# Optimization experiments

Hardware: AMD Instinct MI355X
Metric: run time of the kernel (lower is better)

## Reference

```python
import jax, jax.numpy as jnp
import numpy as np

B, L, D, H = 2, 2048, 2048, 16
DH = D // H

def setup_inputs() -> dict:
    key = jax.random.key(0)
    ks = jax.random.split(key, 7)
    q = jax.random.normal(ks[0], (B, L, D), dtype=jnp.float32)
    k = jax.random.normal(ks[1], (B, L, D), dtype=jnp.float32)
    v = jax.random.normal(ks[2], (B, L, D), dtype=jnp.float32)
    # causal mask: True means masked (matches torch masked_fill semantics)
    attn_mask = jnp.triu(jnp.ones((L, L), dtype=bool), k=1)[None, None, :, :]
    scale = 0.02
    wq = jax.random.normal(ks[3], (D, D), dtype=jnp.float32) * scale
    wk = jax.random.normal(ks[4], (D, D), dtype=jnp.float32) * scale
    wv = jax.random.normal(ks[5], (D, D), dtype=jnp.float32) * scale
    wo = jax.random.normal(ks[6], (D, D), dtype=jnp.float32) * scale
    return {"q": q, "k": k, "v": v, "attn_mask": attn_mask,
            "wq": wq, "wk": wk, "wv": wv, "wo": wo}

def _split_heads(x):
    b, l, _ = x.shape
    return x.reshape(b, l, H, DH).transpose(0, 2, 1, 3)  # [B,H,L,DH]

def reference(q, k, v, attn_mask, wq, wk, wv, wo):
    # torch Linear: y = x @ W.T (bias=False)
    qh = _split_heads(q @ wq.T)
    kh = _split_heads(k @ wk.T)
    vh = _split_heads(v @ wv.T)
    scale = 1.0 / np.sqrt(DH).astype(np.float32)
    scores = jnp.einsum('bhqd,bhkd->bhqk', qh, kh) * scale
    neg = jnp.finfo(scores.dtype).min
    scores = jnp.where(attn_mask, neg, scores)
    attn = jax.nn.softmax(scores, axis=-1)
    ctx = jnp.einsum('bhqk,bhkd->bhqd', attn, vh)
    ctx = ctx.transpose(0, 2, 1, 3).reshape(q.shape[0], q.shape[1], D)
    return ctx @ wo.T
```

## Files before the change

kernel.cpp:

```cpp
#include <hip/hip_runtime.h>

#define B_  2
#define L_  2048
#define D_  2048
#define H_  16
#define DH_ 128
#define K_  2048

typedef __attribute__((ext_vector_type(8))) short bf16x8;
typedef __attribute__((ext_vector_type(4))) float f32x4;
typedef __attribute__((ext_vector_type(4))) float float4v;
typedef __attribute__((ext_vector_type(8))) unsigned short u16x8;
typedef __attribute__((ext_vector_type(4))) unsigned short u16x4;

__device__ __forceinline__ unsigned short f2bf(float f) {
  unsigned u = __builtin_bit_cast(unsigned, f);
  u += 0x7fffu + ((u >> 16) & 1u);
  return (unsigned short)(u >> 16);
}

typedef __attribute__((address_space(3))) unsigned int lds_uint;
typedef __attribute__((address_space(1))) const unsigned int glob_uint;
__device__ __forceinline__ void gld16(const void* g, void* l) {
  __builtin_amdgcn_global_load_lds((glob_uint*)g, (lds_uint*)l, 16, 0, 0);
}

#define BAR() do { asm volatile("" ::: "memory"); __builtin_amdgcn_s_barrier(); asm volatile("" ::: "memory"); } while (0)
#define VMCNT(n) asm volatile("s_waitcnt vmcnt(" #n ")" ::: "memory")

__global__ void cvt_all(const float* __restrict__ wq, const float* __restrict__ wk,
                        const float* __restrict__ wv, const float* __restrict__ wo,
                        const float* __restrict__ q, const float* __restrict__ k,
                        const float* __restrict__ v, unsigned short* __restrict__ ws,
                        int nacts) {
  const size_t DD = (size_t)D_ * D_;
  const size_t BLD = (size_t)B_ * L_ * D_;
  const int z = blockIdx.z;
  const float* src;
  unsigned short* dst;
  size_t nelem;
  if (z < 4) {
    src = (z == 0) ? wq : (z == 1) ? wk : (z == 2) ? wv : wo;
    dst = ws + (size_t)z * DD;
    nelem = DD;
  } else {
    if (z - 4 >= nacts) return;
    src = (z == 4) ? q : (z == 5) ? k : v;
    dst = ws + 4 * DD + (size_t)(z - 4) * BLD;
    nelem = BLD;
  }
  size_t i = ((size_t)blockIdx.x * 256 + threadIdx.x) * 8;
  if (i >= nelem) return;
  float4v x0 = *(const float4v*)(src + i);
  float4v x1 = *(const float4v*)(src + i + 4);
  u16x8 p;
  p[0]=f2bf(x0[0]); p[1]=f2bf(x0[1]); p[2]=f2bf(x0[2]); p[3]=f2bf(x0[3]);
  p[4]=f2bf(x1[0]); p[5]=f2bf(x1[1]); p[6]=f2bf(x1[2]); p[7]=f2bf(x1[3]);
  *(u16x8*)(dst + i) = p;
}

template <int KIND>
__global__ __launch_bounds__(512, 2) void gemm8(
    const unsigned short* __restrict__ a0, const unsigned short* __restrict__ a1,
    const unsigned short* __restrict__ a2,
    const unsigned short* __restrict__ w0, const unsigned short* __restrict__ w1,
    const unsigned short* __restrict__ w2,
    unsigned short* __restrict__ Qh, unsigned short* __restrict__ Kh,
    unsigned short* __restrict__ Vt, float* __restrict__ OF) {
  __shared__ unsigned short smem[3 * 24576];

  const int lin = blockIdx.x + 32 * (blockIdx.y + 8 * blockIdx.z);
  const int cpx = KIND ? 32 : 96;
  const int s = (lin & 7) * cpx + (lin >> 3);
  const int mt = s & 31;
  const int r_ = s >> 5;
  const int ntile = KIND ? r_ : (r_ & 7);
  const int z = KIND ? 0 : (r_ >> 3);

  const unsigned short* A = KIND ? a0 : (z == 0 ? a0 : z == 1 ? a1 : a2);
  const unsigned short* W = KIND ? w0 : (z == 0 ? w0 : z == 1 ? w1 : w2);
  const int mode = KIND ? 2 : (z == 2 ? 1 : 0);

  const int bm0 = mt * 128;
  const int bn0 = ntile * 256;

  const int tid = threadIdx.x;
  const int wid = tid >> 6, lane = tid & 63;
  const int wr = wid >> 2, wc = wid & 3;
  const int l15 = lane & 15, l4 = lane >> 4;

  const unsigned short* gsrc[6];
  int ldst[6];
  {
#pragma unroll
    for (int i = 0; i < 2; ++i) {
      const int c = i * 512 + tid, r = c >> 3, s0 = c & 7;
      gsrc[i] = A + (size_t)(bm0 + r) * K_ + ((s0 ^ (r & 7)) << 3);
      ldst[i] = c * 8;
    }
#pragma unroll
    for (int u = 0; u < 2; ++u)
#pragma unroll
      for (int i = 0; i < 2; ++i) {
        const int c = i * 512 + tid, r = c >> 3, s0 = c & 7;
        gsrc[2 + u * 2 + i] = W + (size_t)(bn0 + u * 128 + r) * K_ + ((s0 ^ (r & 7)) << 3);
        ldst[2 + u * 2 + i] = 8192 + (u * 1024 + c) * 8;
      }
  }
#define STAGE(idx, p) do { gld16(gsrc[idx], &smem[(p) * 24576 + ldst[idx]]); gsrc[idx] += 64; } while (0)

  int offA[4][2], offB[4][2];
#pragma unroll
  for (int mf = 0; mf < 4; ++mf)
#pragma unroll
    for (int ks = 0; ks < 2; ++ks) {
      const int row = wr * 64 + mf * 16 + l15;
      const int ch = ks * 4 + l4;
      offA[mf][ks] = row * 64 + ((ch ^ (row & 7)) << 3);
    }
#pragma unroll
  for (int nf = 0; nf < 4; ++nf)
#pragma unroll
    for (int ks = 0; ks < 2; ++ks) {
      const int rowb = wc * 64 + nf * 16 + l15;
      const int ch = ks * 4 + l4;
      offB[nf][ks] = 8192 + rowb * 64 + ((ch ^ (rowb & 7)) << 3);
    }

  f32x4 acc[4][4];
#pragma unroll
  for (int m = 0; m < 4; ++m)
#pragma unroll
    for (int n = 0; n < 4; ++n) { f32x4 zz = {0.f, 0.f, 0.f, 0.f}; acc[m][n] = zz; }

  STAGE(0, 0); STAGE(1, 0); STAGE(2, 0); STAGE(3, 0); STAGE(4, 0); STAGE(5, 0);
  STAGE(0, 1); STAGE(1, 1); STAGE(2, 1); STAGE(3, 1); STAGE(4, 1); STAGE(5, 1);
  VMCNT(6);
  BAR();

  int p = 0;
  for (int t = 0; t < 32; ++t) {
    int p2 = p + 2; if (p2 >= 3) p2 -= 3;
    const unsigned short* bA = &smem[p * 24576];
    bf16x8 af[4][2], bfr[4][2];
#pragma unroll
    for (int mf = 0; mf < 4; ++mf)
#pragma unroll
      for (int ks = 0; ks < 2; ++ks)
        af[mf][ks] = *(const bf16x8*)&bA[offA[mf][ks]];
#pragma unroll
    for (int nf = 0; nf < 4; ++nf)
#pragma unroll
      for (int ks = 0; ks < 2; ++ks)
        bfr[nf][ks] = *(const bf16x8*)&bA[offB[nf][ks]];
    if (t < 30) { STAGE(0, p2); STAGE(1, p2); STAGE(2, p2); STAGE(3, p2); STAGE(4, p2); STAGE(5, p2); }
    __builtin_amdgcn_s_setprio(1);
#pragma unroll
    for (int mf = 0; mf < 4; ++mf)
#pragma unroll
      for (int nf = 0; nf < 4; ++nf)
#pragma unroll
        for (int ks = 0; ks < 2; ++ks)
          acc[mf][nf] = __builtin_amdgcn_mfma_f32_16x16x32_bf16(af[mf][ks], bfr[nf][ks], acc[mf][nf], 0, 0, 0);
    __builtin_amdgcn_s_setprio(0);
    if (t < 30) { VMCNT(6); } else { VMCNT(0); }
    BAR();
    p = (p == 2) ? 0 : p + 1;
  }
#undef STAGE

  if (mode == 0) {
    unsigned short* O = (z == 0) ? Qh : Kh;
#pragma unroll
    for (int mf = 0; mf < 4; ++mf) {
      const int rr = bm0 + wr * 64 + mf * 16 + l4 * 4;
#pragma unroll
      for (int nf = 0; nf < 4; ++nf) {
        const int cc = bn0 + wc * 64 + nf * 16 + l15;
        const int h = cc >> 7, dh = cc & 127;
#pragma unroll
        for (int j = 0; j < 4; ++j) {
          const int r2 = rr + j;
          O[((size_t)((r2 >> 11) * H_ + h) * L_ + (r2 & 2047)) * DH_ + dh] = f2bf(acc[mf][nf][j]);
        }
      }
    }
  } else if (mode == 1) {
    unsigned short* T = smem;
#pragma unroll
    for (int mf = 0; mf < 4; ++mf) {
      const int rl = wr * 64 + mf * 16 + l4 * 4;
#pragma unroll
      for (int nf = 0; nf < 4; ++nf) {
        const int cl = wc * 64 + nf * 16 + l15;
        u16x4 vv;
#pragma unroll
        for (int j = 0; j < 4; ++j) vv[j] = f2bf(acc[mf][nf][j]);
        *(u16x4*)&T[cl * 136 + rl] = vv;
      }
    }
    __syncthreads();
    const int b = bm0 >> 11, lbase = bm0 & 2047;
#pragma unroll
    for (int it = 0; it < 8; ++it) {
      const int idx = it * 512 + tid;
      const int rT = idx >> 4, cT = idx & 15;
      u16x8 val = *(const u16x8*)&T[rT * 136 + cT * 8];
      const int n = bn0 + rT, h = n >> 7, dh = n & 127;
      *(u16x8*)&Vt[((size_t)(b * H_ + h) * DH_ + dh) * L_ + lbase + cT * 8] = val;
    }
  } else {
#pragma unroll
    for (int mf = 0; mf < 4; ++mf) {
      const int rr = bm0 + wr * 64 + mf * 16 + l4 * 4;
#pragma unroll
      for (int nf = 0; nf < 4; ++nf) {
        const int cc = bn0 + wc * 64 + nf * 16 + l15;
#pragma unroll
        for (int j = 0; j < 4; ++j) OF[(size_t)(rr + j) * D_ + cc] = acc[mf][nf][j];
      }
    }
  }
}

__global__ __launch_bounds__(256, 2) void proj_gemm_f32a(
    const float* __restrict__ q, const float* __restrict__ k, const float* __restrict__ v,
    const unsigned short* __restrict__ wqb, const unsigned short* __restrict__ wkb,
    const unsigned short* __restrict__ wvb,
    unsigned short* __restrict__ Qh, unsigned short* __restrict__ Kh,
    unsigned short* __restrict__ Vt) {
  __shared__ unsigned short smem[128 * 136];
  unsigned short* As = smem;
  unsigned short* Bs = smem + 128 * 64;

  const int z = blockIdx.z;
  const float* A = (z == 0) ? q : (z == 1) ? k : v;
  const unsigned short* W = (z == 0) ? wqb : (z == 1) ? wkb : wvb;

  const int tid = threadIdx.x;
  const int wave = tid >> 6, lane = tid & 63;
  const int wr = wave >> 1, wc = wave & 1;
  const int bm0 = blockIdx.x * 128;
  const int bn0 = blockIdx.y * 128;
  const int l15 = lane & 15, l4 = lane >> 4;

  f32x4 acc[4][4];
#pragma unroll
  for (int m = 0; m < 4; m++)
#pragma unroll
    for (int n = 0; n < 4; n++) { f32x4 zz = {0.f, 0.f, 0.f, 0.f}; acc[m][n] = zz; }

  for (int k0 = 0; k0 < K_; k0 += 64) {
#pragma unroll
    for (int it = 0; it < 4; ++it) {
      const int base = it * 256 + wave * 64;
      const int ch = base + lane;
      const int r = ch >> 3, c = ch & 7;
      gld16(W + (size_t)(bn0 + r) * K_ + (k0 + c * 8), Bs + base * 8);
    }
#pragma unroll
    for (int it = 0; it < 4; ++it) {
      const int ch = it * 256 + tid;
      const int r = ch >> 3, c = ch & 7;
      const float* g = A + (size_t)(bm0 + r) * K_ + (k0 + c * 8);
      float4v x0 = *(const float4v*)g;
      float4v x1 = *(const float4v*)(g + 4);
      u16x8 pp;
      pp[0]=f2bf(x0[0]); pp[1]=f2bf(x0[1]); pp[2]=f2bf(x0[2]); pp[3]=f2bf(x0[3]);
      pp[4]=f2bf(x1[0]); pp[5]=f2bf(x1[1]); pp[6]=f2bf(x1[2]); pp[7]=f2bf(x1[3]);
      *(u16x8*)&As[ch * 8] = pp;
    }
    __syncthreads();
#pragma unroll
    for (int ks = 0; ks < 2; ++ks) {
      const int kc = ks * 32 + l4 * 8;
      bf16x8 af[4], bfr[4];
#pragma unroll
      for (int m = 0; m < 4; m++) af[m] = *(const bf16x8*)&As[(wr * 64 + m * 16 + l15) * 64 + kc];
#pragma unroll
      for (int n = 0; n < 4; n++) bfr[n] = *(const bf16x8*)&Bs[(wc * 64 + n * 16 + l15) * 64 + kc];
#pragma unroll
      for (int m = 0; m < 4; m++)
#pragma unroll
        for (int n = 0; n < 4; n++)
          acc[m][n] = __builtin_amdgcn_mfma_f32_16x16x32_bf16(af[m], bfr[n], acc[m][n], 0, 0, 0);
    }
    __syncthreads();
  }

  if (z < 2) {
    unsigned short* O = (z == 0) ? Qh : Kh;
#pragma unroll
    for (int m = 0; m < 4; m++) {
      const int rr = bm0 + wr * 64 + m * 16 + l4 * 4;
#pragma unroll
      for (int n = 0; n < 4; n++) {
        const int cc = bn0 + wc * 64 + n * 16 + l15;
        const int h = cc >> 7, dh = cc & 127;
#pragma unroll
        for (int j = 0; j < 4; j++) {
          const int r2 = rr + j;
          O[((size_t)((r2 >> 11) * H_ + h) * L_ + (r2 & 2047)) * DH_ + dh] = f2bf(acc[m][n][j]);
        }
      }
    }
  } else {
    __syncthreads();
    unsigned short* T = smem;
#pragma unroll
    for (int m = 0; m < 4; m++)
#pragma unroll
      for (int n = 0; n < 4; n++) {
        const int cl = wc * 64 + n * 16 + l15;
        const int rl = wr * 64 + m * 16 + l4 * 4;
#pragma unroll
        for (int j = 0; j < 4; j++) T[cl * 136 + rl + j] = f2bf(acc[m][n][j]);
      }
    __syncthreads();
    const int b = bm0 >> 11, lbase = bm0 & 2047;
    const int hb = bn0 >> 7;
#pragma unroll
    for (int it = 0; it < 8; ++it) {
      const int idx = it * 256 + tid;
      const int dhl = idx >> 4, c = idx & 15;
      u16x8 val = *(const u16x8*)&T[dhl * 136 + c * 8];
      *(u16x8*)&Vt[((size_t)(b * H_ + hb) * DH_ + dhl) * L_ + lbase + c * 8] = val;
    }
  }
}

#define SCALE_ 0.08838834764831845f

__global__ __launch_bounds__(512, 2) void attn_kernel(
    const unsigned short* __restrict__ Qh, const unsigned short* __restrict__ Kh,
    const unsigned short* __restrict__ Vt, unsigned short* __restrict__ ctx) {
  __shared__ unsigned short Ks[128 * 128];
  __shared__ unsigned short Vs[128 * 128];
  __shared__ unsigned short Ps[8][16 * 128];

  const int pair = blockIdx.x, bh = blockIdx.y;
  const size_t hoff = (size_t)bh * L_ * DH_;
  const unsigned short* Qp = Qh + hoff;
  const unsigned short* Kp = Kh + hoff;
  const unsigned short* Vp = Vt + hoff;

  const int tid = threadIdx.x, wave = tid >> 6, lane = tid & 63;
  const int l15 = lane & 15, l4 = lane >> 4;
  const int b = bh >> 4, h = bh & 15;

#pragma unroll 1
  for (int p = 0; p < 2; ++p) {
    const int qt = p ? (15 - pair) : pair;
    const int ntiles = qt + 1;

    bf16x8 qf[4];
    {
      const int qrow = qt * 128 + wave * 16 + l15;
#pragma unroll
      for (int s = 0; s < 4; s++)
        qf[s] = *(const bf16x8*)&Qp[(size_t)qrow * DH_ + s * 32 + l4 * 8];
    }

    f32x4 o[8];
#pragma unroll
    for (int df = 0; df < 8; df++) { f32x4 zz = {0.f, 0.f, 0.f, 0.f}; o[df] = zz; }
    float m_r[4] = {-1e30f, -1e30f, -1e30f, -1e30f};
    float l_r[4] = {0.f, 0.f, 0.f, 0.f};

    for (int kt = 0; kt < ntiles; ++kt) {
#pragma unroll
      for (int it = 0; it < 4; ++it) {
        const int ch = it * 512 + tid;
        const int r = ch >> 4, s = ch & 15;
        gld16(Kp + (size_t)(kt * 128 + r) * DH_ + ((s ^ (r & 7)) * 8), (unsigned short*)Ks + ch * 8);
      }
#pragma unroll
      for (int it = 0; it < 4; ++it) {
        const int ch = it * 512 + tid;
        const int r = ch >> 4, s = ch & 15;
        gld16(Vp + (size_t)r * L_ + kt * 128 + ((s ^ (r & 7)) * 8), (unsigned short*)Vs + ch * 8);
      }
      __syncthreads();

      f32x4 sa[8];
#pragma unroll
      for (int f = 0; f < 8; f++) { f32x4 zz = {0.f, 0.f, 0.f, 0.f}; sa[f] = zz; }
      __builtin_amdgcn_s_setprio(1);
#pragma unroll
      for (int ks = 0; ks < 4; ++ks) {
        const int c = ks * 4 + l4;
#pragma unroll
        for (int f = 0; f < 8; ++f) {
          const int n = f * 16 + l15;
          bf16x8 kf = *(const bf16x8*)&Ks[n * 128 + ((c ^ (n & 7)) * 8)];
          sa[f] = __builtin_amdgcn_mfma_f32_16x16x32_bf16(qf[ks], kf, sa[f], 0, 0, 0);
        }
      }
      __builtin_amdgcn_s_setprio(0);

      const bool last = (kt == qt);
#pragma unroll
      for (int f = 0; f < 8; f++) {
        const int kg = kt * 128 + f * 16 + l15;
#pragma unroll
        for (int j = 0; j < 4; j++) {
          float t = sa[f][j] * SCALE_;
          if (last && kg > qt * 128 + wave * 16 + l4 * 4 + j) t = -1e30f;
          sa[f][j] = t;
        }
      }

#pragma unroll
      for (int j = 0; j < 4; j++) {
        float mx = fmaxf(fmaxf(fmaxf(sa[0][j], sa[1][j]), fmaxf(sa[2][j], sa[3][j])),
                         fmaxf(fmaxf(sa[4][j], sa[5][j]), fmaxf(sa[6][j], sa[7][j])));
#pragma unroll
        for (int d = 1; d < 16; d <<= 1) mx = fmaxf(mx, __shfl_xor(mx, d));
        const float mnew = fmaxf(m_r[j], mx);
        const float alpha = __expf(m_r[j] - mnew);
        float rs = 0.f;
        const int row = l4 * 4 + j;
#pragma unroll
        for (int f = 0; f < 8; f++) {
          float pp = __expf(sa[f][j] - mnew);
          rs += pp;
          const int col = f * 16 + l15;
          const int c = col >> 3;
          Ps[wave][row * 128 + ((c ^ (row & 7)) * 8) + (col & 7)] = f2bf(pp);
        }
#pragma unroll
        for (int d = 1; d < 16; d <<= 1) rs += __shfl_xor(rs, d);
        l_r[j] = l_r[j] * alpha + rs;
        m_r[j] = mnew;
#pragma unroll
        for (int df = 0; df < 8; df++) o[df][j] *= alpha;
      }

      __builtin_amdgcn_s_setprio(1);
#pragma unroll
      for (int ksl = 0; ksl < 4; ++ksl) {
        const int pc = ksl * 4 + l4;
        bf16x8 pf = *(const bf16x8*)&Ps[wave][l15 * 128 + ((pc ^ (l15 & 7)) * 8)];
#pragma unroll
        for (int df = 0; df < 8; ++df) {
          const int vr = df * 16 + l15;
          bf16x8 vf = *(const bf16x8*)&Vs[vr * 128 + ((pc ^ (vr & 7)) * 8)];
          o[df] = __builtin_amdgcn_mfma_f32_16x16x32_bf16(pf, vf, o[df], 0, 0, 0);
        }
      }
      __builtin_amdgcn_s_setprio(0);
      __syncthreads();
    }

#pragma unroll
    for (int j = 0; j < 4; j++) {
      const float inv = 1.0f / l_r[j];
      const int lq = qt * 128 + wave * 16 + l4 * 4 + j;
      const size_t rowb = ((size_t)(b * L_ + lq)) * D_ + h * DH_;
#pragma unroll
      for (int df = 0; df < 8; ++df)
        ctx[rowb + df * 16 + l15] = f2bf(o[df][j] * inv);
    }
  }
}

extern "C" void kernel_launch(void* const* d_in, const int* in_sizes, int n_in,
                              void* d_out, int out_size, void* d_ws, size_t ws_size,
                              hipStream_t stream) {
  const float* q  = (const float*)d_in[0];
  const float* k  = (const float*)d_in[1];
  const float* v  = (const float*)d_in[2];
  const float* wq = (const float*)d_in[4];
  const float* wk = (const float*)d_in[5];
  const float* wv = (const float*)d_in[6];
  const float* wo = (const float*)d_in[7];

  const size_t DD = (size_t)D_ * D_;
  const size_t BLD = (size_t)B_ * L_ * D_;
  unsigned short* ws  = (unsigned short*)d_ws;
  unsigned short* wqb = ws;
  unsigned short* wkb = wqb + DD;
  unsigned short* wvb = wkb + DD;
  unsigned short* wob = wvb + DD;

  const size_t need_full = (4 * DD + 7 * BLD) * 2;

  if (ws_size >= need_full) {
    unsigned short* qb  = wob + DD;
    unsigned short* kb  = qb + BLD;
    unsigned short* vb  = kb + BLD;
    unsigned short* QhP = vb + BLD;
    unsigned short* KhP = QhP + BLD;
    unsigned short* VtP = KhP + BLD;
    unsigned short* ctx = VtP + BLD;

    cvt_all<<<dim3(4096, 1, 7), 256, 0, stream>>>(wq, wk, wv, wo, q, k, v, ws, 3);
    gemm8<0><<<dim3(32, 8, 3), 512, 0, stream>>>(qb, kb, vb, wqb, wkb, wvb, QhP, KhP, VtP, nullptr);
    attn_kernel<<<dim3(8, 32), 512, 0, stream>>>(QhP, KhP, VtP, ctx);
    gemm8<1><<<dim3(32, 8, 1), 512, 0, stream>>>(ctx, nullptr, nullptr, wob, nullptr, nullptr,
                                                 nullptr, nullptr, nullptr, (float*)d_out);
  } else {
    unsigned short* QhP = wob + DD;
    unsigned short* KhP = QhP + BLD;
    unsigned short* VtP = KhP + BLD;
    unsigned short* ctx = VtP + BLD;

    cvt_all<<<dim3(4096, 1, 4), 256, 0, stream>>>(wq, wk, wv, wo, q, k, v, ws, 0);
    proj_gemm_f32a<<<dim3(32, 16, 3), 256, 0, stream>>>(q, k, v, wqb, wkb, wvb, QhP, KhP, VtP);
    attn_kernel<<<dim3(8, 32), 512, 0, stream>>>(QhP, KhP, VtP, ctx);
    gemm8<1><<<dim3(32, 8, 1), 512, 0, stream>>>(ctx, nullptr, nullptr, wob, nullptr, nullptr,
                                                 nullptr, nullptr, nullptr, (float*)d_out);
  }
}
```

Baseline: 286.5 us.

## Use 256x256 tiles with double buffering for QKV projection GEMM

Replaces the templated 128x256 triple-buffered projection GEMM with a dedicated 256x256-tile kernel that uses two LDS buffers of 64 KB each. Each wave now computes an 8x4 grid of MFMA fragments, loading A fragments inside the loop to limit register pressure. The V transpose epilogue is split into two halves so it fits in shared memory. The larger tile raises arithmetic intensity and cuts global traffic, but it halves the grid to 384 blocks, needs more registers for the bigger accumulator, and waits on VMCNT(0) each iteration, which reduces load/compute overlap. The output projection moves into its own non-templated kernel.

```diff
diff --git a/kernel.cpp b/kernel.cpp
--- a/kernel.cpp
+++ b/kernel.cpp
@@ -59,27 +59,165 @@
   *(u16x8*)(dst + i) = p;
 }
 
-template <int KIND>
-__global__ __launch_bounds__(512, 2) void gemm8(
+__global__ __launch_bounds__(512, 2) void gemm256(
     const unsigned short* __restrict__ a0, const unsigned short* __restrict__ a1,
     const unsigned short* __restrict__ a2,
     const unsigned short* __restrict__ w0, const unsigned short* __restrict__ w1,
     const unsigned short* __restrict__ w2,
     unsigned short* __restrict__ Qh, unsigned short* __restrict__ Kh,
-    unsigned short* __restrict__ Vt, float* __restrict__ OF) {
+    unsigned short* __restrict__ Vt) {
+  __shared__ unsigned short smem[2 * 32768];
+
+  const int lin = blockIdx.x + 16 * (blockIdx.y + 8 * blockIdx.z);
+  const int s = (lin & 7) * 48 + (lin >> 3);
+  const int mt = s & 15;
+  const int r_ = s >> 4;
+  const int ntile = r_ & 7;
+  const int z = r_ >> 3;
+
+  const unsigned short* A = (z == 0) ? a0 : (z == 1) ? a1 : a2;
+  const unsigned short* W = (z == 0) ? w0 : (z == 1) ? w1 : w2;
+
+  const int bm0 = mt * 256;
+  const int bn0 = ntile * 256;
+
+  const int tid = threadIdx.x;
+  const int wid = tid >> 6, lane = tid & 63;
+  const int wr = wid >> 2;
+  const int wc = wid & 3;
+  const int l15 = lane & 15, l4 = lane >> 4;
+
+  const unsigned short* gsrc[8];
+  int ldst[8];
+#pragma unroll
+  for (int i = 0; i < 4; ++i) {
+    const int c = i * 512 + tid, r = c >> 3, s0 = c & 7;
+    gsrc[i] = A + (size_t)(bm0 + r) * K_ + ((s0 ^ (r & 7)) << 3);
+    ldst[i] = c * 8;
+    gsrc[4 + i] = W + (size_t)(bn0 + r) * K_ + ((s0 ^ (r & 7)) << 3);
+    ldst[4 + i] = 16384 + c * 8;
+  }
+#define STAGE(idx, p) do { gld16(gsrc[idx], &smem[(p) * 32768 + ldst[idx]]); gsrc[idx] += 64; } while (0)
+
+  int offA[8][2], offB[4][2];
+#pragma unroll
+  for (int mf = 0; mf < 8; ++mf)
+#pragma unroll
+    for (int ks = 0; ks < 2; ++ks) {
+      const int row = wr * 128 + mf * 16 + l15;
+      const int ch = ks * 4 + l4;
+      offA[mf][ks] = row * 64 + ((ch ^ (row & 7)) << 3);
+    }
+#pragma unroll
+  for (int nf = 0; nf < 4; ++nf)
+#pragma unroll
+    for (int ks = 0; ks < 2; ++ks) {
+      const int rowb = wc * 64 + nf * 16 + l15;
+      const int ch = ks * 4 + l4;
+      offB[nf][ks] = 16384 + rowb * 64 + ((ch ^ (rowb & 7)) << 3);
+    }
+
+  f32x4 acc[8][4];
+#pragma unroll
+  for (int m = 0; m < 8; ++m)
+#pragma unroll
+    for (int n = 0; n < 4; ++n) { f32x4 zz = {0.f, 0.f, 0.f, 0.f}; acc[m][n] = zz; }
+
+  STAGE(0, 0); STAGE(1, 0); STAGE(2, 0); STAGE(3, 0);
+  STAGE(4, 0); STAGE(5, 0); STAGE(6, 0); STAGE(7, 0);
+  VMCNT(0);
+  BAR();
+
+  int p = 0;
+  for (int t = 0; t < 32; ++t) {
+    const int p2 = p ^ 1;
+    if (t < 31) {
+      STAGE(0, p2); STAGE(1, p2); STAGE(2, p2); STAGE(3, p2);
+      STAGE(4, p2); STAGE(5, p2); STAGE(6, p2); STAGE(7, p2);
+    }
+    const unsigned short* bA = &smem[p * 32768];
+    bf16x8 bfr[4][2];
+#pragma unroll
+    for (int nf = 0; nf < 4; ++nf)
+#pragma unroll
+      for (int ks = 0; ks < 2; ++ks)
+        bfr[nf][ks] = *(const bf16x8*)&bA[offB[nf][ks]];
+    __builtin_amdgcn_s_setprio(1);
+#pragma unroll
+    for (int mf = 0; mf < 8; ++mf) {
+      bf16x8 a0f = *(const bf16x8*)&bA[offA[mf][0]];
+      bf16x8 a1f = *(const bf16x8*)&bA[offA[mf][1]];
+#pragma unroll
+      for (int nf = 0; nf < 4; ++nf) {
+        acc[mf][nf] = __builtin_amdgcn_mfma_f32_16x16x32_bf16(a0f, bfr[nf][0], acc[mf][nf], 0, 0, 0);
+        acc[mf][nf] = __builtin_amdgcn_mfma_f32_16x16x32_bf16(a1f, bfr[nf][1], acc[mf][nf], 0, 0, 0);
+      }
+    }
+    __builtin_amdgcn_s_setprio(0);
+    VMCNT(0);
+    BAR();
+    p = p2;
+  }
+#undef STAGE
+
+  if (z < 2) {
+    unsigned short* O = (z == 0) ? Qh : Kh;
+#pragma unroll
+    for (int mf = 0; mf < 8; ++mf) {
+      const int rr = bm0 + wr * 128 + mf * 16 + l4 * 4;
+#pragma unroll
+      for (int nf = 0; nf < 4; ++nf) {
+        const int cc = bn0 + wc * 64 + nf * 16 + l15;
+        const int h = cc >> 7, dh = cc & 127;
+#pragma unroll
+        for (int j = 0; j < 4; ++j) {
+          const int r2 = rr + j;
+          O[((size_t)((r2 >> 11) * H_ + h) * L_ + (r2 & 2047)) * DH_ + dh] = f2bf(acc[mf][nf][j]);
+        }
+      }
+    }
+  } else {
+    unsigned short* T = smem;
+    const int b = bm0 >> 11, lb = bm0 & 2047;
+#pragma unroll 1
+    for (int half = 0; half < 2; ++half) {
+      if (half) __syncthreads();
+      if (wr == half) {
+#pragma unroll
+        for (int mf = 0; mf < 8; ++mf) {
+          const int rl = mf * 16 + l4 * 4;
+#pragma unroll
+          for (int nf = 0; nf < 4; ++nf) {
+            const int cl = wc * 64 + nf * 16 + l15;
+            u16x4 vv;
+#pragma unroll
+            for (int j = 0; j < 4; ++j) vv[j] = f2bf(acc[mf][nf][j]);
+            *(u16x4*)&T[cl * 144 + rl] = vv;
+          }
+        }
+      }
+      __syncthreads();
+#pragma unroll
+      for (int it = 0; it < 8; ++it) {
+        const int idx = it * 512 + tid;
+        const int rT = idx >> 4, cT = idx & 15;
+        u16x8 val = *(const u16x8*)&T[rT * 144 + cT * 8];
+        const int n = bn0 + rT, h = n >> 7, dh = n & 127;
+        *(u16x8*)&Vt[((size_t)(b * H_ + h) * DH_ + dh) * L_ + lb + half * 128 + cT * 8] = val;
+      }
+    }
+  }
+}
+
+__global__ __launch_bounds__(512, 2) void gemm8o(
+    const unsigned short* __restrict__ A, const unsigned short* __restrict__ W,
+    float* __restrict__ OF) {
   __shared__ unsigned short smem[3 * 24576];
 
-  const int lin = blockIdx.x + 32 * (blockIdx.y + 8 * blockIdx.z);
-  const int cpx = KIND ? 32 : 96;
-  const int s = (lin & 7) * cpx + (lin >> 3);
+  const int lin = blockIdx.x + 32 * blockIdx.y;
+  const int s = (lin & 7) * 32 + (lin >> 3);
   const int mt = s & 31;
-  const int r_ = s >> 5;
-  const int ntile = KIND ? r_ : (r_ & 7);
-  const int z = KIND ? 0 : (r_ >> 3);
-
-  const unsigned short* A = KIND ? a0 : (z == 0 ? a0 : z == 1 ? a1 : a2);
-  const unsigned short* W = KIND ? w0 : (z == 0 ? w0 : z == 1 ? w1 : w2);
-  const int mode = KIND ? 2 : (z == 2 ? 1 : 0);
+  const int ntile = s >> 5;
 
   const int bm0 = mt * 128;
   const int bn0 = ntile * 256;
@@ -169,56 +307,14 @@
   }
 #undef STAGE
 
-  if (mode == 0) {
-    unsigned short* O = (z == 0) ? Qh : Kh;
-#pragma unroll
-    for (int mf = 0; mf < 4; ++mf) {
-      const int rr = bm0 + wr * 64 + mf * 16 + l4 * 4;
-#pragma unroll
-      for (int nf = 0; nf < 4; ++nf) {
-        const int cc = bn0 + wc * 64 + nf * 16 + l15;
-        const int h = cc >> 7, dh = cc & 127;
-#pragma unroll
-        for (int j = 0; j < 4; ++j) {
-          const int r2 = rr + j;
-          O[((size_t)((r2 >> 11) * H_ + h) * L_ + (r2 & 2047)) * DH_ + dh] = f2bf(acc[mf][nf][j]);
-        }
-      }
-    }
-  } else if (mode == 1) {
-    unsigned short* T = smem;
-#pragma unroll
-    for (int mf = 0; mf < 4; ++mf) {
-      const int rl = wr * 64 + mf * 16 + l4 * 4;
-#pragma unroll
-      for (int nf = 0; nf < 4; ++nf) {
-        const int cl = wc * 64 + nf * 16 + l15;
-        u16x4 vv;
-#pragma unroll
-        for (int j = 0; j < 4; ++j) vv[j] = f2bf(acc[mf][nf][j]);
-        *(u16x4*)&T[cl * 136 + rl] = vv;
-      }
-    }
-    __syncthreads();
-    const int b = bm0 >> 11, lbase = bm0 & 2047;
-#pragma unroll
-    for (int it = 0; it < 8; ++it) {
-      const int idx = it * 512 + tid;
-      const int rT = idx >> 4, cT = idx & 15;
-      u16x8 val = *(const u16x8*)&T[rT * 136 + cT * 8];
-      const int n = bn0 + rT, h = n >> 7, dh = n & 127;
-      *(u16x8*)&Vt[((size_t)(b * H_ + h) * DH_ + dh) * L_ + lbase + cT * 8] = val;
-    }
-  } else {
-#pragma unroll
-    for (int mf = 0; mf < 4; ++mf) {
-      const int rr = bm0 + wr * 64 + mf * 16 + l4 * 4;
-#pragma unroll
-      for (int nf = 0; nf < 4; ++nf) {
-        const int cc = bn0 + wc * 64 + nf * 16 + l15;
-#pragma unroll
-        for (int j = 0; j < 4; ++j) OF[(size_t)(rr + j) * D_ + cc] = acc[mf][nf][j];
-      }
+#pragma unroll
+  for (int mf = 0; mf < 4; ++mf) {
+    const int rr = bm0 + wr * 64 + mf * 16 + l4 * 4;
+#pragma unroll
+    for (int nf = 0; nf < 4; ++nf) {
+      const int cc = bn0 + wc * 64 + nf * 16 + l15;
+#pragma unroll
+      for (int j = 0; j < 4; ++j) OF[(size_t)(rr + j) * D_ + cc] = acc[mf][nf][j];
     }
   }
 }
@@ -495,10 +591,9 @@
     unsigned short* ctx = VtP + BLD;
 
     cvt_all<<<dim3(4096, 1, 7), 256, 0, stream>>>(wq, wk, wv, wo, q, k, v, ws, 3);
-    gemm8<0><<<dim3(32, 8, 3), 512, 0, stream>>>(qb, kb, vb, wqb, wkb, wvb, QhP, KhP, VtP, nullptr);
+    gemm256<<<dim3(16, 8, 3), 512, 0, stream>>>(qb, kb, vb, wqb, wkb, wvb, QhP, KhP, VtP);
     attn_kernel<<<dim3(8, 32), 512, 0, stream>>>(QhP, KhP, VtP, ctx);
-    gemm8<1><<<dim3(32, 8, 1), 512, 0, stream>>>(ctx, nullptr, nullptr, wob, nullptr, nullptr,
-                                                 nullptr, nullptr, nullptr, (float*)d_out);
+    gemm8o<<<dim3(32, 8), 512, 0, stream>>>(ctx, wob, (float*)d_out);
   } else {
     unsigned short* QhP = wob + DD;
     unsigned short* KhP = QhP + BLD;
@@ -508,7 +603,6 @@
     cvt_all<<<dim3(4096, 1, 4), 256, 0, stream>>>(wq, wk, wv, wo, q, k, v, ws, 0);
     proj_gemm_f32a<<<dim3(32, 16, 3), 256, 0, stream>>>(q, k, v, wqb, wkb, wvb, QhP, KhP, VtP);
     attn_kernel<<<dim3(8, 32), 512, 0, stream>>>(QhP, KhP, VtP, ctx);
-    gemm8<1><<<dim3(32, 8, 1), 512, 0, stream>>>(ctx, nullptr, nullptr, wob, nullptr, nullptr,
-                                                 nullptr, nullptr, nullptr, (float*)d_out);
-  }
-}
+    gemm8o<<<dim3(32, 8), 512, 0, stream>>>(ctx, wob, (float*)d_out);
+  }
+}
```

New measurement: 289.7 us. About the same (+1.1%).
